# Kernel optimization log

Measured on AMD Instinct MI355X. Metric: run time of the kernel, lower is better.

The kernel has to match this reference:

```python
import jax, jax.numpy as jnp
import numpy as np
import math

DM, DP, P = 1024, 128, 256
B, S = 8, 4096

def setup_inputs() -> dict:
    key = jax.random.key(0)
    ks = jax.random.split(key, 7)
    sd = lambda fan_in: 1.0 / math.sqrt(fan_in)
    return {
        "x": jax.random.normal(ks[0], (B, S, DM), jnp.float32),
        "prim_embeds": jax.random.normal(ks[1], (P, DP), jnp.float32),
        "Wq": jax.random.normal(ks[2], (DP, DM), jnp.float32) * sd(DM),
        "Wk": jax.random.normal(ks[3], (DP, DP), jnp.float32) * sd(DP),
        "Wv": jax.random.normal(ks[4], (DP, DP), jnp.float32) * sd(DP),
        "Wo": jax.random.normal(ks[5], (DM, DP), jnp.float32) * sd(DP),
        "gate_w": jax.random.normal(ks[6], (1, DM), jnp.float32) * sd(DM),
        "gate_b": jnp.zeros((1,), jnp.float32),
    }

def reference(x, prim_embeds, Wq, Wk, Wv, Wo, gate_w, gate_b):
    # q: [B,S,dp]; k,v: [P,dp]
    q = jnp.einsum('bsm,pm->bsp', x, Wq)          # p here = d_prim
    k = prim_embeds @ Wk.T                         # [P, dp]
    v = prim_embeds @ Wv.T                         # [P, dp]
    scale = 1.0 / math.sqrt(q.shape[-1])
    scores = jnp.einsum('bsd,pd->bsp', q, k) * scale  # [B,S,P]
    attn = jax.nn.softmax(scores, axis=-1)
    ctx = jnp.einsum('bsp,pd->bsd', attn, v)       # [B,S,dp]
    out = jnp.einsum('bsd,md->bsm', ctx, Wo)       # [B,S,dm]
    gate = jax.nn.sigmoid(jnp.einsum('bsm,om->bso', x, gate_w) + gate_b)  # [B,S,1]
    return gate * out
```

## Files before the change

kernel.cpp:

```cpp
#include <hip/hip_runtime.h>
#include <hip/hip_bf16.h>

typedef unsigned short ushort_t;
typedef __attribute__((ext_vector_type(8))) short short8;
typedef __attribute__((ext_vector_type(8))) unsigned short ushort8;
typedef __attribute__((ext_vector_type(4))) float f32x4;

#define MFMA16(a,b,c) __builtin_amdgcn_mfma_f32_16x16x32_bf16((a),(b),(c),0,0,0)

__device__ __forceinline__ ushort_t f2bf(float f) {
  unsigned int u = __builtin_bit_cast(unsigned int, f);
  u += 0x7FFFu + ((u >> 16) & 1u);
  return (ushort_t)(u >> 16);
}
__device__ __forceinline__ unsigned int pack2bf(float a, float b) {
  unsigned int ua = __builtin_bit_cast(unsigned int, a);
  unsigned int ub = __builtin_bit_cast(unsigned int, b);
  ua += 0x7FFFu + ((ua >> 16) & 1u);
  ub += 0x7FFFu + ((ub >> 16) & 1u);
  return (ua >> 16) | (ub & 0xFFFF0000u);
}

#define DMd 1024
#define DPd 128
#define PPd 256

#define KWQ_OFF 0
#define KWQ_SIZE (8*17*4*512)
#define VWO_OFF KWQ_SIZE
#define VWO_SIZE (64*8*512)
#define KV_BYTE_OFF ((size_t)(KWQ_SIZE + VWO_SIZE) * 2)

__global__ void prep1_kernel(const float* __restrict__ prim, const float* __restrict__ Wk,
                             const float* __restrict__ Wv, ushort_t* __restrict__ ws) {
  float* kf = (float*)((char*)ws + KV_BYTE_OFF);
  float* vf = kf + 32768;
  int idx = blockIdx.x * 256 + threadIdx.x;
  int mat = idx >> 15, rem = idx & 32767;
  int p = rem >> 7, d = rem & 127;
  const float4* pr = (const float4*)(prim + p * 128);
  const float4* wr = (const float4*)((mat ? Wv : Wk) + d * 128);
  float s0 = 0.f, s1 = 0.f;
  #pragma unroll
  for (int j = 0; j < 32; j += 2) {
    float4 a = pr[j], b = wr[j];
    s0 += a.x*b.x + a.y*b.y + a.z*b.z + a.w*b.w;
    float4 a2 = pr[j+1], b2 = wr[j+1];
    s1 += a2.x*b2.x + a2.y*b2.y + a2.z*b2.z + a2.w*b2.w;
  }
  (mat ? vf : kf)[rem] = s0 + s1;
}

__global__ void prep2_kernel(const float* __restrict__ Wq, const float* __restrict__ Wo,
                             const float* __restrict__ gate_w, ushort_t* __restrict__ ws) {
  const float* kf = (const float*)((const char*)ws + KV_BYTE_OFF);
  const float* vf = kf + 32768;
  const int b = blockIdx.x, t = threadIdx.x;
  if (b < 68) {
    const int p  = (b >> 2) * 16 + (t >> 4);
    const int m0 = (b & 3) * 256 + (t & 15) * 16;
    float acc[16];
    #pragma unroll
    for (int j = 0; j < 16; ++j) acc[j] = 0.f;
    if (p < 256) {
      const float* kp = kf + p * 128;
      for (int d = 0; d < 128; ++d) {
        float kv = kp[d];
        const float4* wr = (const float4*)(Wq + (size_t)d * 1024 + m0);
        #pragma unroll
        for (int q = 0; q < 4; ++q) {
          float4 w = wr[q];
          acc[q*4+0] += kv * w.x; acc[q*4+1] += kv * w.y;
          acc[q*4+2] += kv * w.z; acc[q*4+3] += kv * w.w;
        }
      }
    } else if (p == 256) {
      #pragma unroll
      for (int j = 0; j < 16; ++j) acc[j] = gate_w[m0 + j];
    }
    const int ct = p >> 4, l16p = p & 15;
    const int c = m0 >> 7, k4 = (m0 >> 5) & 3, q0 = (m0 >> 3) & 3;
    ushort8 u0, u1;
    #pragma unroll
    for (int j = 0; j < 8; ++j) { u0[j] = f2bf(acc[j]); u1[j] = f2bf(acc[8+j]); }
    size_t base = ((size_t)(c * 17 + ct) * 4 + k4) * 512;
    *(ushort8*)&ws[KWQ_OFF + base + (size_t)(q0 * 16 + l16p) * 8]       = u0;
    *(ushort8*)&ws[KWQ_OFF + base + (size_t)((q0 + 1) * 16 + l16p) * 8] = u1;
  } else {
    __shared__ float vs[16 * 128];
    const int bb = b - 68;
    const int p0 = (bb >> 2) * 16;
    const int m  = (bb & 3) * 256 + t;
    {
      int row = t >> 4, col = (t & 15) * 8;
      const float4* src = (const float4*)(vf + (p0 + row) * 128 + col);
      float4 a0 = src[0], a1 = src[1];
      *(float4*)&vs[row * 128 + col]     = a0;
      *(float4*)&vs[row * 128 + col + 4] = a1;
    }
    __syncthreads();
    float acc[16];
    #pragma unroll
    for (int j = 0; j < 16; ++j) acc[j] = 0.f;
    const float4* wr = (const float4*)(Wo + (size_t)m * 128);
    for (int d4 = 0; d4 < 32; ++d4) {
      float4 w = wr[d4];
      #pragma unroll
      for (int pp = 0; pp < 16; ++pp) {
        float4 v4 = *(const float4*)&vs[pp * 128 + d4 * 4];
        acc[pp] += w.x*v4.x + w.y*v4.y + w.z*v4.z + w.w*v4.w;
      }
    }
    const int ctg = m >> 4, l16m = m & 15;
    ushort8 u0, u1;
    #pragma unroll
    for (int j = 0; j < 8; ++j) { u0[j] = f2bf(acc[j]); u1[j] = f2bf(acc[8+j]); }
    const int pA = p0, pB = p0 + 8;
    *(ushort8*)&ws[VWO_OFF + ((size_t)(ctg*8 + (pA>>5))*512) + (size_t)(((pA>>3)&3)*16 + l16m)*8] = u0;
    *(ushort8*)&ws[VWO_OFF + ((size_t)(ctg*8 + (pB>>5))*512) + (size_t)(((pB>>3)&3)*16 + l16m)*8] = u1;
  }
}

#define LDX 136
#define LDSLAB 264

__global__ __launch_bounds__(256, 4) void fused_kernel(
    const float* __restrict__ x, const float* __restrict__ gate_b,
    const ushort_t* __restrict__ ws, float* __restrict__ out)
{
  __shared__ __align__(16) char smem[2 * 32 * LDX * 2 + 32 * 4 * 4 * 2 + 32 * 4];
  ushort_t* xt0      = (ushort_t*)smem;
  ushort_t* xt1      = xt0 + 32 * LDX;
  ushort_t* slab     = (ushort_t*)smem;
  float*    pmax     = (float*)(smem + 2 * 32 * LDX * 2);
  float*    psum     = pmax + 128;
  float*    gate_lds = psum + 128;

  const int t = threadIdx.x, wid = t >> 6, lane = t & 63;
  const int quad = lane >> 4, l16 = lane & 15;
  const int tok0 = blockIdx.x * 32;

  f32x4 acc[2][5];
  #pragma unroll
  for (int rt = 0; rt < 2; ++rt)
    #pragma unroll
    for (int ctl = 0; ctl < 5; ++ctl) acc[rt][ctl] = (f32x4){0.f,0.f,0.f,0.f};

  #pragma unroll
  for (int i = 0; i < 4; ++i) {
    int flat = i * 1024 + t * 4;
    int row = flat >> 7, col = flat & 127;
    float4 fv = *(const float4*)(x + (size_t)(tok0 + row) * 1024 + col);
    unsigned int pk0 = pack2bf(fv.x, fv.y), pk1 = pack2bf(fv.z, fv.w);
    *(unsigned long long*)&xt0[row * LDX + col] =
        (unsigned long long)pk0 | ((unsigned long long)pk1 << 32);
  }
  __syncthreads();

  for (int c = 0; c < 8; ++c) {
    ushort_t* cur = (c & 1) ? xt1 : xt0;
    ushort_t* nxt = (c & 1) ? xt0 : xt1;
    float4 fv[4];
    if (c < 7) {
      #pragma unroll
      for (int i = 0; i < 4; ++i) {
        int flat = i * 1024 + t * 4;
        int row = flat >> 7, col = flat & 127;
        fv[i] = *(const float4*)(x + (size_t)(tok0 + row) * 1024 + (c + 1) * 128 + col);
      }
    }
    #pragma unroll
    for (int k4 = 0; k4 < 4; ++k4) {
      short8 a[2];
      #pragma unroll
      for (int rt = 0; rt < 2; ++rt)
        a[rt] = *(const short8*)&cur[(rt * 16 + l16) * LDX + k4 * 32 + quad * 8];
      #pragma unroll
      for (int ctl = 0; ctl < 5; ++ctl) {
        if (ctl == 4 && wid != 3) continue;
        const int ct = wid * 4 + ctl;
        short8 bfr = *(const short8*)&ws[KWQ_OFF +
            ((size_t)(c * 17 + ct) * 4 + k4) * 512 + (size_t)lane * 8];
        #pragma unroll
        for (int rt = 0; rt < 2; ++rt) acc[rt][ctl] = MFMA16(a[rt], bfr, acc[rt][ctl]);
      }
    }
    if (c < 7) {
      #pragma unroll
      for (int i = 0; i < 4; ++i) {
        int flat = i * 1024 + t * 4;
        int row = flat >> 7, col = flat & 127;
        unsigned int pk0 = pack2bf(fv[i].x, fv[i].y), pk1 = pack2bf(fv[i].z, fv[i].w);
        *(unsigned long long*)&nxt[row * LDX + col] =
            (unsigned long long)pk0 | ((unsigned long long)pk1 << 32);
      }
      __syncthreads();
    }
  }

  const float SC = 0.08838834764831845f * 1.44269504088896f;
  float Mx[2][4];
  #pragma unroll
  for (int rt = 0; rt < 2; ++rt)
    #pragma unroll
    for (int r = 0; r < 4; ++r) {
      float m = acc[rt][0][r];
      #pragma unroll
      for (int ctl = 1; ctl < 4; ++ctl) m = fmaxf(m, acc[rt][ctl][r]);
      #pragma unroll
      for (int msk = 1; msk < 16; msk <<= 1) m = fmaxf(m, __shfl_xor(m, msk, 64));
      Mx[rt][r] = m;
    }
  if (l16 == 0) {
    #pragma unroll
    for (int rt = 0; rt < 2; ++rt)
      #pragma unroll
      for (int r = 0; r < 4; ++r)
        pmax[(rt * 16 + quad * 4 + r) * 4 + wid] = Mx[rt][r];
  }
  __syncthreads();
  float Mf[2][4];
  #pragma unroll
  for (int rt = 0; rt < 2; ++rt)
    #pragma unroll
    for (int r = 0; r < 4; ++r) {
      f32x4 pm = *(f32x4*)&pmax[(rt * 16 + quad * 4 + r) * 4];
      Mf[rt][r] = fmaxf(fmaxf(pm[0], pm[1]), fmaxf(pm[2], pm[3]));
    }
  float Sm[2][4];
  #pragma unroll
  for (int rt = 0; rt < 2; ++rt)
    #pragma unroll
    for (int r = 0; r < 4; ++r) Sm[rt][r] = 0.f;
  #pragma unroll
  for (int rt = 0; rt < 2; ++rt)
    #pragma unroll
    for (int ctl = 0; ctl < 4; ++ctl)
      #pragma unroll
      for (int r = 0; r < 4; ++r) {
        float e = exp2f((acc[rt][ctl][r] - Mf[rt][r]) * SC);
        acc[rt][ctl][r] = e;
        Sm[rt][r] += e;
      }
  #pragma unroll
  for (int rt = 0; rt < 2; ++rt)
    #pragma unroll
    for (int r = 0; r < 4; ++r) {
      #pragma unroll
      for (int msk = 1; msk < 16; msk <<= 1) Sm[rt][r] += __shfl_xor(Sm[rt][r], msk, 64);
    }
  if (l16 == 0) {
    #pragma unroll
    for (int rt = 0; rt < 2; ++rt)
      #pragma unroll
      for (int r = 0; r < 4; ++r)
        psum[(rt * 16 + quad * 4 + r) * 4 + wid] = Sm[rt][r];
    if (wid == 3) {
      float gb = gate_b[0];
      #pragma unroll
      for (int rt = 0; rt < 2; ++rt)
        #pragma unroll
        for (int r = 0; r < 4; ++r) {
          float lg = acc[rt][4][r] + gb;
          gate_lds[rt * 16 + quad * 4 + r] = 1.f / (1.f + __expf(-lg));
        }
    }
  }
  __syncthreads();
  float scl[2][4];
  #pragma unroll
  for (int rt = 0; rt < 2; ++rt)
    #pragma unroll
    for (int r = 0; r < 4; ++r) {
      f32x4 ps = *(f32x4*)&psum[(rt * 16 + quad * 4 + r) * 4];
      float g = gate_lds[rt * 16 + quad * 4 + r];
      scl[rt][r] = g / (ps[0] + ps[1] + ps[2] + ps[3]);
    }

  #pragma unroll
  for (int rt = 0; rt < 2; ++rt)
    #pragma unroll
    for (int ctl = 0; ctl < 4; ++ctl)
      #pragma unroll
      for (int r = 0; r < 4; ++r)
        slab[(rt * 16 + quad * 4 + r) * LDSLAB + (wid * 4 + ctl) * 16 + l16] =
            f2bf(acc[rt][ctl][r] * scl[rt][r]);
  __syncthreads();

  short8 af[2][8];
  #pragma unroll
  for (int rt = 0; rt < 2; ++rt)
    #pragma unroll
    for (int k8 = 0; k8 < 8; ++k8)
      af[rt][k8] = *(const short8*)&slab[(rt * 16 + l16) * LDSLAB + k8 * 32 + quad * 8];

  const int n0 = wid * 256;
  for (int nt = 0; nt < 16; ++nt) {
    const int ctg = (n0 >> 4) + nt;
    short8 bf[8];
    #pragma unroll
    for (int k8 = 0; k8 < 8; ++k8)
      bf[k8] = *(const short8*)&ws[VWO_OFF + ((size_t)(ctg * 8 + k8) * 512) + (size_t)lane * 8];
    f32x4 oa[2];
    #pragma unroll
    for (int rt = 0; rt < 2; ++rt) oa[rt] = (f32x4){0.f,0.f,0.f,0.f};
    #pragma unroll
    for (int rt = 0; rt < 2; ++rt)
      #pragma unroll
      for (int k8 = 0; k8 < 8; ++k8)
        oa[rt] = MFMA16(af[rt][k8], bf[k8], oa[rt]);
    #pragma unroll
    for (int rt = 0; rt < 2; ++rt)
      #pragma unroll
      for (int r = 0; r < 4; ++r)
        __builtin_nontemporal_store(oa[rt][r],
            &out[(size_t)(tok0 + rt * 16 + quad * 4 + r) * 1024 + n0 + nt * 16 + l16]);
  }
}

extern "C" void kernel_launch(void* const* d_in, const int* in_sizes, int n_in,
                              void* d_out, int out_size, void* d_ws, size_t ws_size,
                              hipStream_t stream) {
  const float* x    = (const float*)d_in[0];
  const float* prim = (const float*)d_in[1];
  const float* Wq   = (const float*)d_in[2];
  const float* Wk   = (const float*)d_in[3];
  const float* Wv   = (const float*)d_in[4];
  const float* Wo   = (const float*)d_in[5];
  const float* gw   = (const float*)d_in[6];
  const float* gb   = (const float*)d_in[7];
  float* out = (float*)d_out;
  ushort_t* ws = (ushort_t*)d_ws;

  prep1_kernel<<<256, 256, 0, stream>>>(prim, Wk, Wv, ws);
  prep2_kernel<<<132, 256, 0, stream>>>(Wq, Wo, gw, ws);
  fused_kernel<<<1024, 256, 0, stream>>>(x, gb, ws, out);
}
```

Baseline: 328.0 us.

## Restructure prep kernels and double-buffer Wo-fragment loads in output GEMM

prep1 now stages the Wk/Wv weight matrix and two prim rows in shared memory and writes V transposed. prep2 uses more, smaller blocks with coalesced float4 reads of Wq and V^T, and each thread now produces 8 outputs. In the fused kernel, the output projection loop ping-pongs two register buffers of B fragments so the next tile's loads overlap the current MFMAs, and launch bounds drop to 2 waves per EU to leave room for the extra registers. The risks are higher register pressure and lower occupancy in the main kernel.

```diff
diff --git a/kernel.cpp b/kernel.cpp
--- a/kernel.cpp
+++ b/kernel.cpp
@@ -31,100 +31,129 @@
 #define VWO_SIZE (64*8*512)
 #define KV_BYTE_OFF ((size_t)(KWQ_SIZE + VWO_SIZE) * 2)
 
-__global__ void prep1_kernel(const float* __restrict__ prim, const float* __restrict__ Wk,
-                             const float* __restrict__ Wv, ushort_t* __restrict__ ws) {
+__global__ __launch_bounds__(256) void prep1_kernel(
+    const float* __restrict__ prim, const float* __restrict__ Wk,
+    const float* __restrict__ Wv, ushort_t* __restrict__ ws) {
+  __shared__ __align__(16) float Wl[128 * 132];
+  __shared__ __align__(16) float pl[2 * 128];
+  const int t = threadIdx.x;
+  const int mat = blockIdx.x & 1;
+  const int p0 = (blockIdx.x >> 1) * 2;
+  const float* W = mat ? Wv : Wk;
+  #pragma unroll
+  for (int i = 0; i < 16; ++i) {
+    int w = (i * 256 + t) * 4;
+    int row = w >> 7, col = w & 127;
+    *(float4*)&Wl[row * 132 + col] = *(const float4*)(W + w);
+  }
+  if (t < 64) {
+    int row = t >> 5, col = (t & 31) * 4;
+    *(float4*)&pl[row * 128 + col] = *(const float4*)(prim + (p0 + row) * 128 + col);
+  }
+  __syncthreads();
+  const int d = t & 127, slot = t >> 7;
+  float a0 = 0.f, a1 = 0.f, a2 = 0.f, a3 = 0.f;
+  #pragma unroll
+  for (int j = 0; j < 128; j += 4) {
+    float4 w4 = *(const float4*)&Wl[d * 132 + j];
+    float4 p4 = *(const float4*)&pl[slot * 128 + j];
+    a0 += w4.x * p4.x; a1 += w4.y * p4.y; a2 += w4.z * p4.z; a3 += w4.w * p4.w;
+  }
+  float r = (a0 + a1) + (a2 + a3);
   float* kf = (float*)((char*)ws + KV_BYTE_OFF);
-  float* vf = kf + 32768;
-  int idx = blockIdx.x * 256 + threadIdx.x;
-  int mat = idx >> 15, rem = idx & 32767;
-  int p = rem >> 7, d = rem & 127;
-  const float4* pr = (const float4*)(prim + p * 128);
-  const float4* wr = (const float4*)((mat ? Wv : Wk) + d * 128);
-  float s0 = 0.f, s1 = 0.f;
-  #pragma unroll
-  for (int j = 0; j < 32; j += 2) {
-    float4 a = pr[j], b = wr[j];
-    s0 += a.x*b.x + a.y*b.y + a.z*b.z + a.w*b.w;
-    float4 a2 = pr[j+1], b2 = wr[j+1];
-    s1 += a2.x*b2.x + a2.y*b2.y + a2.z*b2.z + a2.w*b2.w;
-  }
-  (mat ? vf : kf)[rem] = s0 + s1;
-}
-
-__global__ void prep2_kernel(const float* __restrict__ Wq, const float* __restrict__ Wo,
-                             const float* __restrict__ gate_w, ushort_t* __restrict__ ws) {
+  float* vT = kf + 32768;
+  if (mat == 0) kf[(p0 + slot) * 128 + d] = r;
+  else          vT[d * 256 + p0 + slot] = r;
+}
+
+__global__ __launch_bounds__(256) void prep2_kernel(
+    const float* __restrict__ Wq, const float* __restrict__ Wo,
+    const float* __restrict__ gate_w, ushort_t* __restrict__ ws) {
   const float* kf = (const float*)((const char*)ws + KV_BYTE_OFF);
-  const float* vf = kf + 32768;
+  const float* vT = kf + 32768;
+  __shared__ __align__(16) float tile[8 * 128];
   const int b = blockIdx.x, t = threadIdx.x;
-  if (b < 68) {
-    const int p  = (b >> 2) * 16 + (t >> 4);
-    const int m0 = (b & 3) * 256 + (t & 15) * 16;
-    float acc[16];
-    #pragma unroll
-    for (int j = 0; j < 16; ++j) acc[j] = 0.f;
-    if (p < 256) {
-      const float* kp = kf + p * 128;
-      for (int d = 0; d < 128; ++d) {
-        float kv = kp[d];
-        const float4* wr = (const float4*)(Wq + (size_t)d * 1024 + m0);
-        #pragma unroll
-        for (int q = 0; q < 4; ++q) {
-          float4 w = wr[q];
-          acc[q*4+0] += kv * w.x; acc[q*4+1] += kv * w.y;
-          acc[q*4+2] += kv * w.z; acc[q*4+3] += kv * w.w;
-        }
+  float acc[8];
+  #pragma unroll
+  for (int j = 0; j < 8; ++j) acc[j] = 0.f;
+  if (b < 136) {
+    const int pt = b >> 2, ms = b & 3;
+    const int p0 = pt * 8;
+    const int p  = p0 + (t >> 5);
+    const int m0 = ms * 256 + (t & 31) * 8;
+    if (p0 < 256) {
+      *(float4*)&tile[t * 4] = *(const float4*)(kf + p0 * 128 + t * 4);
+      __syncthreads();
+      const float* kp = &tile[(t >> 5) * 128];
+      for (int d = 0; d < 128; d += 4) {
+        float4 kv = *(const float4*)&kp[d];
+        float4 qa0 = *(const float4*)(Wq + (d + 0) * 1024 + m0);
+        float4 qb0 = *(const float4*)(Wq + (d + 0) * 1024 + m0 + 4);
+        float4 qa1 = *(const float4*)(Wq + (d + 1) * 1024 + m0);
+        float4 qb1 = *(const float4*)(Wq + (d + 1) * 1024 + m0 + 4);
+        float4 qa2 = *(const float4*)(Wq + (d + 2) * 1024 + m0);
+        float4 qb2 = *(const float4*)(Wq + (d + 2) * 1024 + m0 + 4);
+        float4 qa3 = *(const float4*)(Wq + (d + 3) * 1024 + m0);
+        float4 qb3 = *(const float4*)(Wq + (d + 3) * 1024 + m0 + 4);
+        acc[0] += kv.x*qa0.x + kv.y*qa1.x + kv.z*qa2.x + kv.w*qa3.x;
+        acc[1] += kv.x*qa0.y + kv.y*qa1.y + kv.z*qa2.y + kv.w*qa3.y;
+        acc[2] += kv.x*qa0.z + kv.y*qa1.z + kv.z*qa2.z + kv.w*qa3.z;
+        acc[3] += kv.x*qa0.w + kv.y*qa1.w + kv.z*qa2.w + kv.w*qa3.w;
+        acc[4] += kv.x*qb0.x + kv.y*qb1.x + kv.z*qb2.x + kv.w*qb3.x;
+        acc[5] += kv.x*qb0.y + kv.y*qb1.y + kv.z*qb2.y + kv.w*qb3.y;
+        acc[6] += kv.x*qb0.z + kv.y*qb1.z + kv.z*qb2.z + kv.w*qb3.z;
+        acc[7] += kv.x*qb0.w + kv.y*qb1.w + kv.z*qb2.w + kv.w*qb3.w;
       }
     } else if (p == 256) {
       #pragma unroll
-      for (int j = 0; j < 16; ++j) acc[j] = gate_w[m0 + j];
-    }
-    const int ct = p >> 4, l16p = p & 15;
-    const int c = m0 >> 7, k4 = (m0 >> 5) & 3, q0 = (m0 >> 3) & 3;
-    ushort8 u0, u1;
-    #pragma unroll
-    for (int j = 0; j < 8; ++j) { u0[j] = f2bf(acc[j]); u1[j] = f2bf(acc[8+j]); }
-    size_t base = ((size_t)(c * 17 + ct) * 4 + k4) * 512;
-    *(ushort8*)&ws[KWQ_OFF + base + (size_t)(q0 * 16 + l16p) * 8]       = u0;
-    *(ushort8*)&ws[KWQ_OFF + base + (size_t)((q0 + 1) * 16 + l16p) * 8] = u1;
+      for (int j = 0; j < 8; ++j) acc[j] = gate_w[m0 + j];
+    }
+    const int c = m0 >> 7, ct = p >> 4, k4 = (m0 >> 5) & 3;
+    const int row = ((m0 >> 3) & 3) * 16 + (p & 15);
+    ushort8 u;
+    #pragma unroll
+    for (int j = 0; j < 8; ++j) u[j] = f2bf(acc[j]);
+    *(ushort8*)&ws[KWQ_OFF + ((size_t)(c * 17 + ct) * 4 + k4) * 512 + (size_t)row * 8] = u;
   } else {
-    __shared__ float vs[16 * 128];
-    const int bb = b - 68;
-    const int p0 = (bb >> 2) * 16;
-    const int m  = (bb & 3) * 256 + t;
-    {
-      int row = t >> 4, col = (t & 15) * 8;
-      const float4* src = (const float4*)(vf + (p0 + row) * 128 + col);
-      float4 a0 = src[0], a1 = src[1];
-      *(float4*)&vs[row * 128 + col]     = a0;
-      *(float4*)&vs[row * 128 + col + 4] = a1;
-    }
+    const int mb  = b - 136;
+    const int m0t = mb * 8;
+    const int m   = m0t + (t >> 5);
+    const int p8  = (t & 31) * 8;
+    *(float4*)&tile[t * 4] = *(const float4*)(Wo + (size_t)m0t * 128 + t * 4);
     __syncthreads();
-    float acc[16];
-    #pragma unroll
-    for (int j = 0; j < 16; ++j) acc[j] = 0.f;
-    const float4* wr = (const float4*)(Wo + (size_t)m * 128);
-    for (int d4 = 0; d4 < 32; ++d4) {
-      float4 w = wr[d4];
-      #pragma unroll
-      for (int pp = 0; pp < 16; ++pp) {
-        float4 v4 = *(const float4*)&vs[pp * 128 + d4 * 4];
-        acc[pp] += w.x*v4.x + w.y*v4.y + w.z*v4.z + w.w*v4.w;
-      }
-    }
-    const int ctg = m >> 4, l16m = m & 15;
-    ushort8 u0, u1;
-    #pragma unroll
-    for (int j = 0; j < 8; ++j) { u0[j] = f2bf(acc[j]); u1[j] = f2bf(acc[8+j]); }
-    const int pA = p0, pB = p0 + 8;
-    *(ushort8*)&ws[VWO_OFF + ((size_t)(ctg*8 + (pA>>5))*512) + (size_t)(((pA>>3)&3)*16 + l16m)*8] = u0;
-    *(ushort8*)&ws[VWO_OFF + ((size_t)(ctg*8 + (pB>>5))*512) + (size_t)(((pB>>3)&3)*16 + l16m)*8] = u1;
+    const float* wo = &tile[(t >> 5) * 128];
+    for (int d = 0; d < 128; d += 4) {
+      float4 wv = *(const float4*)&wo[d];
+      float4 va0 = *(const float4*)(vT + (d + 0) * 256 + p8);
+      float4 vb0 = *(const float4*)(vT + (d + 0) * 256 + p8 + 4);
+      float4 va1 = *(const float4*)(vT + (d + 1) * 256 + p8);
+      float4 vb1 = *(const float4*)(vT + (d + 1) * 256 + p8 + 4);
+      float4 va2 = *(const float4*)(vT + (d + 2) * 256 + p8);
+      float4 vb2 = *(const float4*)(vT + (d + 2) * 256 + p8 + 4);
+      float4 va3 = *(const float4*)(vT + (d + 3) * 256 + p8);
+      float4 vb3 = *(const float4*)(vT + (d + 3) * 256 + p8 + 4);
+      acc[0] += wv.x*va0.x + wv.y*va1.x + wv.z*va2.x + wv.w*va3.x;
+      acc[1] += wv.x*va0.y + wv.y*va1.y + wv.z*va2.y + wv.w*va3.y;
+      acc[2] += wv.x*va0.z + wv.y*va1.z + wv.z*va2.z + wv.w*va3.z;
+      acc[3] += wv.x*va0.w + wv.y*va1.w + wv.z*va2.w + wv.w*va3.w;
+      acc[4] += wv.x*vb0.x + wv.y*vb1.x + wv.z*vb2.x + wv.w*vb3.x;
+      acc[5] += wv.x*vb0.y + wv.y*vb1.y + wv.z*vb2.y + wv.w*vb3.y;
+      acc[6] += wv.x*vb0.z + wv.y*vb1.z + wv.z*vb2.z + wv.w*vb3.z;
+      acc[7] += wv.x*vb0.w + wv.y*vb1.w + wv.z*vb2.w + wv.w*vb3.w;
+    }
+    const int ctg = m >> 4, k8 = p8 >> 5;
+    const int row = ((p8 >> 3) & 3) * 16 + (m & 15);
+    ushort8 u;
+    #pragma unroll
+    for (int j = 0; j < 8; ++j) u[j] = f2bf(acc[j]);
+    *(ushort8*)&ws[VWO_OFF + ((size_t)(ctg * 8 + k8) * 512) + (size_t)row * 8] = u;
   }
 }
 
 #define LDX 136
 #define LDSLAB 264
 
-__global__ __launch_bounds__(256, 4) void fused_kernel(
+__global__ __launch_bounds__(256, 2) void fused_kernel(
     const float* __restrict__ x, const float* __restrict__ gate_b,
     const ushort_t* __restrict__ ws, float* __restrict__ out)
 {
@@ -295,26 +324,56 @@
       af[rt][k8] = *(const short8*)&slab[(rt * 16 + l16) * LDSLAB + k8 * 32 + quad * 8];
 
   const int n0 = wid * 256;
-  for (int nt = 0; nt < 16; ++nt) {
-    const int ctg = (n0 >> 4) + nt;
-    short8 bf[8];
+  const ushort_t* vb = ws + VWO_OFF + (size_t)(n0 >> 4) * (8 * 512) + (size_t)lane * 8;
+
+  short8 bfA[8], bfB[8];
+  #pragma unroll
+  for (int k8 = 0; k8 < 8; ++k8)
+    bfA[k8] = *(const short8*)&vb[(size_t)k8 * 512];
+
+  #pragma unroll 2
+  for (int ntp = 0; ntp < 8; ++ntp) {
+    const int ntA = ntp * 2, ntB = ntA + 1;
     #pragma unroll
     for (int k8 = 0; k8 < 8; ++k8)
-      bf[k8] = *(const short8*)&ws[VWO_OFF + ((size_t)(ctg * 8 + k8) * 512) + (size_t)lane * 8];
-    f32x4 oa[2];
-    #pragma unroll
-    for (int rt = 0; rt < 2; ++rt) oa[rt] = (f32x4){0.f,0.f,0.f,0.f};
-    #pragma unroll
-    for (int rt = 0; rt < 2; ++rt)
+      bfB[k8] = *(const short8*)&vb[(size_t)(ntB * 8 + k8) * 512];
+    {
+      f32x4 oa[2];
+      #pragma unroll
+      for (int rt = 0; rt < 2; ++rt) oa[rt] = (f32x4){0.f,0.f,0.f,0.f};
+      #pragma unroll
+      for (int rt = 0; rt < 2; ++rt)
+        #pragma unroll
+        for (int k8 = 0; k8 < 8; ++k8)
+          oa[rt] = MFMA16(af[rt][k8], bfA[k8], oa[rt]);
+      #pragma unroll
+      for (int rt = 0; rt < 2; ++rt)
+        #pragma unroll
+        for (int r = 0; r < 4; ++r)
+          __builtin_nontemporal_store(oa[rt][r],
+              &out[(size_t)(tok0 + rt * 16 + quad * 4 + r) * 1024 + n0 + ntA * 16 + l16]);
+    }
+    if (ntp < 7) {
       #pragma unroll
       for (int k8 = 0; k8 < 8; ++k8)
-        oa[rt] = MFMA16(af[rt][k8], bf[k8], oa[rt]);
-    #pragma unroll
-    for (int rt = 0; rt < 2; ++rt)
-      #pragma unroll
-      for (int r = 0; r < 4; ++r)
-        __builtin_nontemporal_store(oa[rt][r],
-            &out[(size_t)(tok0 + rt * 16 + quad * 4 + r) * 1024 + n0 + nt * 16 + l16]);
+        bfA[k8] = *(const short8*)&vb[(size_t)((ntA + 2) * 8 + k8) * 512];
+    }
+    {
+      f32x4 oa[2];
+      #pragma unroll
+      for (int rt = 0; rt < 2; ++rt) oa[rt] = (f32x4){0.f,0.f,0.f,0.f};
+      #pragma unroll
+      for (int rt = 0; rt < 2; ++rt)
+        #pragma unroll
+        for (int k8 = 0; k8 < 8; ++k8)
+          oa[rt] = MFMA16(af[rt][k8], bfB[k8], oa[rt]);
+      #pragma unroll
+      for (int rt = 0; rt < 2; ++rt)
+        #pragma unroll
+        for (int r = 0; r < 4; ++r)
+          __builtin_nontemporal_store(oa[rt][r],
+              &out[(size_t)(tok0 + rt * 16 + quad * 4 + r) * 1024 + n0 + ntB * 16 + l16]);
+    }
   }
 }
 
@@ -333,6 +392,6 @@
   ushort_t* ws = (ushort_t*)d_ws;
 
   prep1_kernel<<<256, 256, 0, stream>>>(prim, Wk, Wv, ws);
-  prep2_kernel<<<132, 256, 0, stream>>>(Wq, Wo, gw, ws);
+  prep2_kernel<<<264, 256, 0, stream>>>(Wq, Wo, gw, ws);
   fused_kernel<<<1024, 256, 0, stream>>>(x, gb, ws, out);
 }
```

New measurement: 348.9 us. +6.4%, slower.
